# Kernel tuning notes

Hardware: AMD Instinct MI355X
Metric: run time of the kernel (lower is better)

## Reference

```python
import jax, jax.numpy as jnp
import numpy as np

B, T, C, H, K = 16, 8192, 256, 256, 7


def setup_inputs() -> dict:
    key = jax.random.key(0)
    ks = jax.random.split(key, 6)
    x = jax.random.normal(ks[0], (B, T, C), dtype=jnp.float32)
    # ragged lengths in [T//2, T]; padding_mask: True = padding (at tail)
    lengths = jax.random.randint(ks[1], (B,), T // 2, T + 1)
    padding_mask = jnp.arange(T)[None, :] >= lengths[:, None]
    w1 = jax.random.normal(ks[2], (H, C, K), dtype=jnp.float32) / np.sqrt(C * K)
    b1 = jnp.zeros((H,), jnp.float32)
    w2 = jax.random.normal(ks[3], (H, H, 3), dtype=jnp.float32) / np.sqrt(H * 3)
    b2 = jnp.zeros((H,), jnp.float32)
    w3 = jax.random.normal(ks[4], (2, H, 1), dtype=jnp.float32) / np.sqrt(H)
    b3 = jnp.zeros((2,), jnp.float32)
    return {"x": x, "padding_mask": padding_mask,
            "w1": w1, "b1": b1, "w2": w2, "b2": b2, "w3": w3, "b3": b3}


def _conv1d(h, w, b, pad):
    # h: (B, Cin, T), w: (Cout, Cin, K) torch OIW layout
    y = jax.lax.conv_general_dilated(h, w, (1,), [(pad, pad)],
                                     dimension_numbers=("NCH", "OIH", "NCH"))
    return y + b[None, :, None]


def _boundary_logits(x, w1, b1, w2, b2, w3, b3):
    # RebornSegmenter.forward (dropout is identity in eval)
    h = jnp.transpose(x, (0, 2, 1))            # (B, C, T)
    h = jax.nn.relu(_conv1d(h, w1, b1, K // 2))
    h = jax.nn.relu(_conv1d(h, w2, b2, 1))
    h = _conv1d(h, w3, b3, 0)                  # (B, 2, T)
    return jnp.transpose(h, (0, 2, 1))         # (B, T, 2)


def _segment_pool(xb, sid):
    # xb: (T, C), sid: (T,) in [0, T] (T == dropped/padding)
    sums = jax.ops.segment_sum(xb, sid, num_segments=T)
    cnt = jax.ops.segment_sum(jnp.ones((T,), xb.dtype), sid, num_segments=T)
    return sums, cnt


def reference(x, padding_mask, w1, b1, w2, b2, w3, b3):
    # pre_segment with deterministic=True (boundary = argmax of conv logits)
    boundary_logits = _boundary_logits(x, w1, b1, w2, b2, w3, b3)
    boundary = jnp.argmax(boundary_logits, axis=-1)            # (B, T)
    is_b = (boundary == 1) & (~padding_mask)
    # token t belongs to segment = number of boundaries in [0..t]
    seg_id = jnp.cumsum(is_b.astype(jnp.int32), axis=1)
    seg_id = jnp.where(padding_mask, T, seg_id)  # out-of-range -> dropped
    sums, cnt = jax.vmap(_segment_pool)(x, seg_id)             # (B,T,C),(B,T)
    # segment mean; empty segments -> 0 (output padded to T segments, jit-safe;
    # torch crops to max segment count, extra columns here are flagged padded)
    new_logits = jnp.where(cnt[..., None] > 0,
                           sums / jnp.maximum(cnt, 1.0)[..., None], 0.0)
    nb = jnp.sum(is_b, axis=1)
    n_valid = jnp.where(jnp.any(~padding_mask, axis=1), nb + 1, 0)
    new_pad = jnp.arange(T)[None, :] >= n_valid[:, None]       # (B, T)
    return new_logits, new_pad
```

## Files before the change

### kernel.cpp

```cpp
#include <hip/hip_runtime.h>
#include <cstdint>
#include <cstddef>

#define BSZ 16
#define T   8192
#define CDIM 256
#define HDIM 256
#define KW  7

constexpr int BT = BSZ * T;
constexpr float TAU = 2e-3f;
constexpr int RCAP = 8192;

typedef __attribute__((ext_vector_type(8))) short short8;
typedef _Float16 half8 __attribute__((ext_vector_type(8)));
typedef __attribute__((ext_vector_type(4))) float f32x4;

constexpr size_t B_W1T  = 0;
constexpr size_t B_W2T  = B_W1T + 1835008;
constexpr size_t B_V    = B_W2T + 786432;
constexpr size_t B_D    = B_V + 1024;
constexpr size_t B_ISB  = B_D + 524288;
constexpr size_t B_SID  = B_ISB + 524288;
constexpr size_t B_SST  = B_SID + 524288;
constexpr size_t B_SEN  = B_SST + 524288;
constexpr size_t B_NV   = B_SEN + 524288;
constexpr size_t B_UCT  = B_NV + 64;
constexpr size_t B_UL   = B_UCT + 16;
constexpr size_t B_ZERO = B_UL + 32768;
constexpr size_t B_W1B  = B_ZERO + 256;
constexpr size_t B_W2B  = B_W1B + 917504;
constexpr size_t B_H1F  = B_W2B + 393216;
constexpr size_t B_DSUM = B_H1F + 25165824;

__device__ __forceinline__ void gl_lds16(const void* g, void* l) {
    __builtin_amdgcn_global_load_lds(
        (const __attribute__((address_space(1))) unsigned int*)g,
        (__attribute__((address_space(3))) unsigned int*)l,
        16, 0, 0);
}

__device__ __forceinline__ unsigned short f16_rne(float f) {
    _Float16 h = (_Float16)f;
    return __builtin_bit_cast(unsigned short, h);
}


__global__ void repack_kernel(const float* __restrict__ w1, const float* __restrict__ w2,
                              const float* __restrict__ w3,
                              float* __restrict__ W1R, float* __restrict__ W2R,
                              float* __restrict__ v,
                              unsigned short* __restrict__ W1bL, unsigned short* __restrict__ W2bL)
{
    int idx = blockIdx.x * blockDim.x + threadIdx.x;
    int stride = gridDim.x * blockDim.x;
    for (int i = idx; i < HDIM * 1792; i += stride) {
        int h = i / 1792, kc = i % 1792, kw = kc >> 8, c = kc & 255;
        W1R[i] = w1[(size_t)h * 1792 + c * 7 + kw];
    }
    for (int i = idx; i < HDIM * 768; i += stride) {
        int h = i / 768, kc = i % 768, kw = kc >> 8, c = kc & 255;
        W2R[i] = w2[(size_t)h * 768 + c * 3 + kw];
    }
    for (int o = idx; o < 4 * 8 * 28 * 512; o += stride) {
        int e = o & 7, lane = (o >> 3) & 63;
        int su = o >> 9;
        int slot = su % 28, rest = su / 28;
        int cc = rest & 7, h0g = rest >> 3;
        int kw = slot >> 2, bq = slot & 3;
        int h = h0g * 64 + lane;
        int c = cc * 32 + bq * 8 + e;
        W1bL[o] = f16_rne(w1[(size_t)h * 1792 + c * 7 + kw]);
    }
    for (int o = idx; o < 4 * 8 * 12 * 512; o += stride) {
        int e = o & 7, lane = (o >> 3) & 63;
        int su = o >> 9;
        int slot = su % 12, rest = su / 12;
        int cc = rest & 7, h0g = rest >> 3;
        int kw = slot >> 2, bq = slot & 3;
        int h = h0g * 64 + lane;
        int c = cc * 32 + bq * 8 + e;
        W2bL[o] = f16_rne(w2[(size_t)h * 768 + c * 3 + kw]);
    }
    if (idx < HDIM) v[idx] = w3[HDIM + idx] - w3[idx];
}

__global__ __launch_bounds__(256) void xcast_kernel(const float* __restrict__ x,
                                                    unsigned short* __restrict__ xt)
{
    int j = blockIdx.x * 256 + threadIdx.x;
    int rin = j & 255, wid = (j >> 8) & 3, cc = (j >> 10) & 7, grp = (j >> 13) & 31, b = j >> 18;
    int t = grp * 256 + rin;
    int c0 = cc * 32 + wid * 8;
    const float* src = x + ((size_t)(b * T + t)) * 256 + c0;
    float4 a = *(const float4*)src;
    float4 bb = *(const float4*)(src + 4);
    short8 o;
    o[0] = (short)f16_rne(a.x); o[1] = (short)f16_rne(a.y);
    o[2] = (short)f16_rne(a.z); o[3] = (short)f16_rne(a.w);
    o[4] = (short)f16_rne(bb.x); o[5] = (short)f16_rne(bb.y);
    o[6] = (short)f16_rne(bb.z); o[7] = (short)f16_rne(bb.w);
    *(short8*)(xt + (size_t)j * 8) = o;
}

__device__ __forceinline__ void c1_stageA(const unsigned short* xt, const unsigned short* zerobuf,
                                          half8* Ab, int b, int t0, int cc, int lane, int wid)
{
    #pragma unroll
    for (int part = 0; part < 5; ++part) {
        int row = part * 64 + lane;
        int t = t0 + row - 3;
        const unsigned short* src = zerobuf;
        if (row < 262 && t >= 0 && t < T) {
            int grp = t >> 8, rin = t & 255;
            src = xt + ((size_t)((((b * 32 + grp) * 8 + cc) * 4 + wid) * 256 + rin)) * 8;
        }
        gl_lds16(src, &Ab[wid * 322 + part * 64]);
    }
}
__device__ __forceinline__ void c1_stageB(const unsigned short* WbL, half8* Bb,
                                          int hcc, int lane, int wid)
{
    #pragma unroll
    for (int s = 0; s < 7; ++s) {
        int slot = wid * 7 + s;
        const unsigned short* src = WbL + ((size_t)(hcc * 28 + slot)) * 512 + lane * 8;
        gl_lds16(src, &Bb[slot * 66]);
    }
}

__global__ __launch_bounds__(256, 3) void conv1_mfma(
    const unsigned short* __restrict__ xt,
    const unsigned short* __restrict__ WbL,
    const float* __restrict__ b1,
    const unsigned short* __restrict__ zerobuf,
    unsigned short* __restrict__ h1t)
{
    __shared__ half8 A8[4 * 322];
    __shared__ half8 B8[28 * 66];
    const int tid = threadIdx.x, lane = tid & 63, wid = tid >> 6;
    const int b  = blockIdx.x >> 5;
    const int grp = blockIdx.x & 31;
    const int t0 = grp << 8;
    const int h0 = blockIdx.y << 6;
    const int q = lane >> 4, l15 = lane & 15;

    f32x4 acc[4][4] = {};

    for (int cc = 0; cc < 8; ++cc) {
        __syncthreads();
        c1_stageA(xt, zerobuf, A8, b, t0, cc, lane, wid);
        c1_stageB(WbL, B8, blockIdx.y * 8 + cc, lane, wid);
        __syncthreads();
        #pragma unroll
        for (int kw = 0; kw < 7; ++kw) {
            half8 ah[4], bh[4];
            const int rbase = wid * 64 + l15 + kw;
            #pragma unroll
            for (int i = 0; i < 4; ++i) ah[i] = A8[q * 322 + rbase + i * 16];
            #pragma unroll
            for (int j = 0; j < 4; ++j) bh[j] = B8[(kw * 4 + q) * 66 + j * 16 + l15];
            #pragma unroll
            for (int i = 0; i < 4; ++i)
                #pragma unroll
                for (int j = 0; j < 4; ++j)
                    acc[i][j] = __builtin_amdgcn_mfma_f32_16x16x32_f16(ah[i], bh[j], acc[i][j], 0, 0, 0);
        }
    }
    #pragma unroll
    for (int j = 0; j < 4; ++j) {
        int h = h0 + j * 16 + l15;
        float bb = b1[h];
        int hcc = h >> 5, hwid = (h >> 3) & 3, he = h & 7;
        size_t hbase = ((size_t)(((b * 32 + grp) * 8 + hcc) * 4 + hwid)) * 2048 + he;
        #pragma unroll
        for (int i = 0; i < 4; ++i) {
            int rb = wid * 64 + i * 16 + q * 4;
            #pragma unroll
            for (int r = 0; r < 4; ++r)
                h1t[hbase + (size_t)(rb + r) * 8] = f16_rne(fmaxf(acc[i][j][r] + bb, 0.f));
        }
    }
}

__device__ __forceinline__ void c2_stageA(const unsigned short* ht, const unsigned short* zerobuf,
                                          half8* Ab, int b, int t0, int cc, int lane, int wid)
{
    #pragma unroll
    for (int part = 0; part < 5; ++part) {
        int row = part * 64 + lane;
        int t = t0 + row - 1;
        const unsigned short* src = zerobuf;
        if (row < 258 && t >= 0 && t < T) {
            int grp = t >> 8, rin = t & 255;
            src = ht + ((size_t)((((b * 32 + grp) * 8 + cc) * 4 + wid) * 256 + rin)) * 8;
        }
        gl_lds16(src, &Ab[wid * 322 + part * 64]);
    }
}
__device__ __forceinline__ void c2_stageB(const unsigned short* WbL, half8* Bb,
                                          int hcc, int lane, int wid)
{
    #pragma unroll
    for (int s = 0; s < 3; ++s) {
        int slot = wid * 3 + s;
        const unsigned short* src = WbL + ((size_t)(hcc * 12 + slot)) * 512 + lane * 8;
        gl_lds16(src, &Bb[slot * 66]);
    }
}

__global__ __launch_bounds__(256, 3) void conv2_mfma(
    const unsigned short* __restrict__ h1t,
    const unsigned short* __restrict__ WbL,
    const float* __restrict__ b2, const float* __restrict__ v,
    const unsigned short* __restrict__ zerobuf,
    float* __restrict__ dlog)
{
    __shared__ half8 A8[4 * 322];
    __shared__ half8 B8[12 * 66];
    const int tid = threadIdx.x, lane = tid & 63, wid = tid >> 6;
    const int b  = blockIdx.x >> 5;
    const int t0 = (blockIdx.x & 31) << 8;
    const int h0 = blockIdx.y << 6;
    const int q = lane >> 4, l15 = lane & 15;

    f32x4 acc[4][4] = {};

    for (int cc = 0; cc < 8; ++cc) {
        __syncthreads();
        c2_stageA(h1t, zerobuf, A8, b, t0, cc, lane, wid);
        c2_stageB(WbL, B8, blockIdx.y * 8 + cc, lane, wid);
        __syncthreads();
        #pragma unroll
        for (int kw = 0; kw < 3; ++kw) {
            half8 ah[4], bh[4];
            const int rbase = wid * 64 + l15 + kw;
            #pragma unroll
            for (int i = 0; i < 4; ++i) ah[i] = A8[q * 322 + rbase + i * 16];
            #pragma unroll
            for (int j = 0; j < 4; ++j) bh[j] = B8[(kw * 4 + q) * 66 + j * 16 + l15];
            #pragma unroll
            for (int i = 0; i < 4; ++i)
                #pragma unroll
                for (int j = 0; j < 4; ++j)
                    acc[i][j] = __builtin_amdgcn_mfma_f32_16x16x32_f16(ah[i], bh[j], acc[i][j], 0, 0, 0);
        }
    }
    float vv[4], bb[4];
    #pragma unroll
    for (int j = 0; j < 4; ++j) {
        int h = h0 + j * 16 + l15;
        vv[j] = v[h]; bb[j] = b2[h];
    }
    #pragma unroll
    for (int i = 0; i < 4; ++i) {
        int tb = t0 + wid * 64 + i * 16 + q * 4;
        #pragma unroll
        for (int r = 0; r < 4; ++r) {
            float s = 0.f;
            #pragma unroll
            for (int j = 0; j < 4; ++j)
                s += fmaxf(acc[i][j][r] + bb[j], 0.f) * vv[j];
            #pragma unroll
            for (int m = 1; m < 16; m <<= 1)
                s += __shfl_xor(s, m, 64);
            if (l15 == 0) atomicAdd(&dlog[b * T + tb + r], s);
        }
    }
}

__global__ void boundary_kernel(const float* __restrict__ d, const int* __restrict__ padmask,
                                const float* __restrict__ b3,
                                int* __restrict__ isb, int* __restrict__ ucount,
                                int* __restrict__ ulist)
{
    int bt = blockIdx.x * 256 + threadIdx.x;
    if (bt >= BT) return;
    int pad = padmask[bt];
    float dd = d[bt] + (b3[1] - b3[0]);
    isb[bt] = (pad == 0 && dd > 0.f) ? 1 : 0;
    if (pad == 0 && fabsf(dd) < TAU) {
        int slot = atomicAdd(ucount, 1);
        if (slot < RCAP) ulist[slot] = bt;
    }
}

__global__ __launch_bounds__(256) void recheck_h1(
    const float* __restrict__ x, const float* __restrict__ W1R,
    const float* __restrict__ b1, const float* __restrict__ zerof,
    const int* __restrict__ ulist, const int* __restrict__ ucount,
    float* __restrict__ h1f)
{
    __shared__ float xs[9 * CDIM];
    int n = *ucount; if (n > RCAP) n = RCAP;
    const int tid = threadIdx.x, lane = tid & 63, wid = tid >> 6;
    const int g = tid >> 4, l = tid & 15;
    const int nit = 4 * n;
    for (int item = blockIdx.x; item < nit; item += gridDim.x) {
        const int li = item >> 2, hc = item & 3;
        const int bt = ulist[li];
        const int b = bt >> 13, t = bt & (T - 1);
        __syncthreads();
        for (int r = wid; r < 9; r += 4) {
            int tt = t + r - 4;
            const float* src = (tt >= 0 && tt < T)
                ? x + (size_t)(b * T + tt) * CDIM + lane * 4 : zerof;
            gl_lds16(src, &xs[r * CDIM]);
        }
        __syncthreads();
        #pragma unroll
        for (int s = 0; s < 4; ++s) {
            const int h = hc * 64 + s * 16 + g;
            const float* wr = &W1R[(size_t)h * 1792];
            double p0 = 0.0, p1 = 0.0, p2 = 0.0;
            #pragma unroll 7
            for (int it = 0; it < 28; ++it) {
                const int e = it * 64 + l * 4;
                float4 w4 = *(const float4*)&wr[e];
                double w0 = (double)w4.x, w1v = (double)w4.y,
                       w2v = (double)w4.z, w3v = (double)w4.w;
                const float* x0 = &xs[e];
                p0 += w0 * (double)x0[0] + w1v * (double)x0[1]
                    + w2v * (double)x0[2] + w3v * (double)x0[3];
                const float* x1 = &xs[256 + e];
                p1 += w0 * (double)x1[0] + w1v * (double)x1[1]
                    + w2v * (double)x1[2] + w3v * (double)x1[3];
                const float* x2 = &xs[512 + e];
                p2 += w0 * (double)x2[0] + w1v * (double)x2[1]
                    + w2v * (double)x2[2] + w3v * (double)x2[3];
            }
            #pragma unroll
            for (int m = 1; m < 16; m <<= 1) {
                p0 += __shfl_xor(p0, m);
                p1 += __shfl_xor(p1, m);
                p2 += __shfl_xor(p2, m);
            }
            if (l == 0) {
                double bb = (double)b1[h];
                double a0 = bb + p0, a1 = bb + p1, a2 = bb + p2;
                float* o = &h1f[(size_t)li * 768];
                o[0 * 256 + h] = (t - 1 >= 0 && a0 > 0.0) ? (float)a0 : 0.f;
                o[1 * 256 + h] = (a1 > 0.0) ? (float)a1 : 0.f;
                o[2 * 256 + h] = (t + 1 < T && a2 > 0.0) ? (float)a2 : 0.f;
            }
        }
    }
}

__global__ __launch_bounds__(256) void recheck_h2(
    const float* __restrict__ h1f, const float* __restrict__ W2R,
    const float* __restrict__ b2, const float* __restrict__ w3,
    const int* __restrict__ ulist, const int* __restrict__ ucount,
    double* __restrict__ dsum)
{
    __shared__ float hs[768];
    __shared__ double red[64];
    int n = *ucount; if (n > RCAP) n = RCAP;
    const int tid = threadIdx.x, lane = tid & 63, wid = tid >> 6;
    const int g = tid >> 4, l = tid & 15;
    const int nit = 4 * n;
    for (int item = blockIdx.x; item < nit; item += gridDim.x) {
        const int li = item >> 2, hc = item & 3;
        __syncthreads();
        if (wid < 3)
            gl_lds16(h1f + (size_t)li * 768 + wid * 256 + lane * 4, &hs[wid * 256]);
        __syncthreads();
        #pragma unroll
        for (int s = 0; s < 4; ++s) {
            const int h = hc * 64 + s * 16 + g;
            const float* wr = &W2R[(size_t)h * 768];
            double c0 = 0.0;
            #pragma unroll
            for (int it = 0; it < 12; ++it) {
                const int e = it * 64 + l * 4;
                float4 w4 = *(const float4*)&wr[e];
                const float* hv = &hs[e];
                c0 += (double)w4.x * (double)hv[0] + (double)w4.y * (double)hv[1]
                    + (double)w4.z * (double)hv[2] + (double)w4.w * (double)hv[3];
            }
            #pragma unroll
            for (int m = 1; m < 16; m <<= 1) c0 += __shfl_xor(c0, m);
            if (l == 0) {
                double acc2 = (double)b2[h] + c0;
                double h2v = acc2 > 0.0 ? acc2 : 0.0;
                double vd = (double)w3[HDIM + h] - (double)w3[h];
                red[s * 16 + g] = vd * h2v;
            }
        }
        __syncthreads();
        if (tid < 32) red[tid] += red[tid + 32];
        __syncthreads();
        if (tid < 16) red[tid] += red[tid + 16];
        __syncthreads();
        if (tid == 0) {
            double ssum = 0.0;
            #pragma unroll
            for (int i = 0; i < 16; ++i) ssum += red[i];
            atomicAdd(&dsum[li], ssum);
        }
    }
}

__global__ void recheck_final(const double* __restrict__ dsum, const float* __restrict__ b3,
                              const int* __restrict__ ulist, const int* __restrict__ ucount,
                              int* __restrict__ isb)
{
    int n = *ucount; if (n > RCAP) n = RCAP;
    int li = blockIdx.x * 256 + threadIdx.x;
    if (li >= n) return;
    double dd = dsum[li] + ((double)b3[1] - (double)b3[0]);
    isb[ulist[li]] = (dd > 0.0) ? 1 : 0;
}

__global__ __launch_bounds__(1024) void scan_kernel(
    const int* __restrict__ isb, const int* __restrict__ padmask,
    int* __restrict__ sid, int* __restrict__ nvalid)
{
    __shared__ int ssum[1024];
    const int b = blockIdx.x, tid = threadIdx.x;
    const int base = b * T;
    int vals[8]; int s = 0;
    #pragma unroll
    for (int i = 0; i < 8; ++i) { vals[i] = isb[base + tid * 8 + i]; s += vals[i]; }
    ssum[tid] = s;
    __syncthreads();
    for (int off = 1; off < 1024; off <<= 1) {
        int add = (tid >= off) ? ssum[tid - off] : 0;
        __syncthreads();
        ssum[tid] += add;
        __syncthreads();
    }
    int run = ssum[tid] - s;
    #pragma unroll
    for (int i = 0; i < 8; ++i) {
        int t = tid * 8 + i;
        run += vals[i];
        sid[base + t] = (padmask[base + t] != 0) ? T : run;
    }
    if (tid == 1023) {
        int nb = ssum[1023];
        nvalid[b] = (padmask[base] == 0) ? (nb + 1) : 0;
    }
}

__global__ void segbounds_kernel(const int* __restrict__ sid, const int* __restrict__ padmask,
                                 int* __restrict__ sst, int* __restrict__ sen)
{
    int bt = blockIdx.x * 256 + threadIdx.x;
    if (bt >= BT) return;
    if (padmask[bt] != 0) return;
    int t = bt & (T - 1);
    int b = bt >> 13;
    int s = sid[bt];
    if (t == 0) {
        if (s < T) sst[b * T + s] = 0;
    } else if (s != sid[bt - 1]) {
        if (s < T) sst[b * T + s] = t;
    }
    bool last = (t == T - 1) || (padmask[bt + 1] != 0);
    if (s < T && (last || sid[bt + 1] != s)) sen[b * T + s] = t + 1;
}

__global__ __launch_bounds__(256) void pool_kernel(
    const float* __restrict__ x, const int* __restrict__ sst,
    const int* __restrict__ sen, const int* __restrict__ nvalid,
    float* __restrict__ out)
{
    int slot = blockIdx.x * 4 + (threadIdx.x >> 6);
    int lane = threadIdx.x & 63;
    int b = slot >> 13;
    int s = slot & (T - 1);
    int nv = nvalid[b];
    float4 res = make_float4(0.f, 0.f, 0.f, 0.f);
    if (s < nv) {
        int st = sst[slot], en = sen[slot];
        if (st >= 0 && en > st) {
            float4 a = make_float4(0.f, 0.f, 0.f, 0.f);
            const float* xp = &x[(size_t)(b * T + st) * CDIM + lane * 4];
            for (int t = st; t < en; ++t) {
                float4 xv = *(const float4*)xp;
                a.x += xv.x; a.y += xv.y; a.z += xv.z; a.w += xv.w;
                xp += CDIM;
            }
            float inv = 1.f / (float)(en - st);
            res = make_float4(a.x * inv, a.y * inv, a.z * inv, a.w * inv);
        }
    }
    *(float4*)&out[(size_t)slot * CDIM + lane * 4] = res;
    if (lane == 0) out[(size_t)BT * CDIM + slot] = (s < nv) ? 0.f : 1.f;
}

extern "C" void kernel_launch(void* const* d_in, const int* in_sizes, int n_in,
                              void* d_out, int out_size, void* d_ws, size_t ws_size,
                              hipStream_t stream)
{
    const float* x  = (const float*)d_in[0];
    const int* padmask = (const int*)d_in[1];
    const float* w1 = (const float*)d_in[2];
    const float* b1 = (const float*)d_in[3];
    const float* w2 = (const float*)d_in[4];
    const float* b2 = (const float*)d_in[5];
    const float* w3 = (const float*)d_in[6];
    const float* b3 = (const float*)d_in[7];

    char* ws = (char*)d_ws;
    float* W1R = (float*)(ws + B_W1T);
    float* W2R = (float*)(ws + B_W2T);
    float* v   = (float*)(ws + B_V);
    float* dlog = (float*)(ws + B_D);
    int* isb = (int*)(ws + B_ISB);
    int* sid = (int*)(ws + B_SID);
    int* sst = (int*)(ws + B_SST);
    int* sen = (int*)(ws + B_SEN);
    int* nv  = (int*)(ws + B_NV);
    int* uct = (int*)(ws + B_UCT);
    int* ul  = (int*)(ws + B_UL);
    unsigned short* zerobuf = (unsigned short*)(ws + B_ZERO);
    unsigned short* W1bL = (unsigned short*)(ws + B_W1B);
    unsigned short* W2bL = (unsigned short*)(ws + B_W2B);
    float* h1f = (float*)(ws + B_H1F);
    double* dsum = (double*)(ws + B_DSUM);

    float* out = (float*)d_out;
    unsigned short* h1t = (unsigned short*)out;
    unsigned short* xt  = h1t + (size_t)BT * 256;

    hipMemsetAsync(dlog, 0, BT * sizeof(float), stream);
    hipMemsetAsync(sst, 0xFF, BT * sizeof(int), stream);
    hipMemsetAsync(sen, 0xFF, BT * sizeof(int), stream);
    hipMemsetAsync(uct, 0, sizeof(int), stream);
    hipMemsetAsync(zerobuf, 0, 256, stream);
    hipMemsetAsync(dsum, 0, RCAP * sizeof(double), stream);

    repack_kernel<<<1024, 256, 0, stream>>>(w1, w2, w3, W1R, W2R, v, W1bL, W2bL);
    xcast_kernel<<<BT * 256 / (8 * 256), 256, 0, stream>>>(x, xt);
    conv1_mfma<<<dim3(BSZ * (T / 256), HDIM / 64), 256, 0, stream>>>(
        xt, W1bL, b1, zerobuf, h1t);
    conv2_mfma<<<dim3(BSZ * (T / 256), HDIM / 64), 256, 0, stream>>>(
        h1t, W2bL, b2, v, zerobuf, dlog);
    boundary_kernel<<<BT / 256, 256, 0, stream>>>(dlog, padmask, b3, isb, uct, ul);
    recheck_h1<<<4096, 256, 0, stream>>>(x, W1R, b1, (const float*)zerobuf, ul, uct, h1f);
    recheck_h2<<<4096, 256, 0, stream>>>(h1f, W2R, b2, w3, ul, uct, dsum);
    recheck_final<<<RCAP / 256, 256, 0, stream>>>(dsum, b3, ul, uct, isb);
    scan_kernel<<<BSZ, 1024, 0, stream>>>(isb, padmask, sid, nv);
    segbounds_kernel<<<BT / 256, 256, 0, stream>>>(sid, padmask, sst, sen);
    pool_kernel<<<BT / 4, 256, 0, stream>>>(x, sst, sen, nv, out);
}
```

Baseline: 586.2 us.

## Load conv weights directly into registers and remap blocks across XCDs

Measured after the change: 613.0 us. 4.6% more time.

```diff
diff --git a/kernel.cpp b/kernel.cpp
--- a/kernel.cpp
+++ b/kernel.cpp
@@ -118,16 +118,6 @@
         gl_lds16(src, &Ab[wid * 322 + part * 64]);
     }
 }
-__device__ __forceinline__ void c1_stageB(const unsigned short* WbL, half8* Bb,
-                                          int hcc, int lane, int wid)
-{
-    #pragma unroll
-    for (int s = 0; s < 7; ++s) {
-        int slot = wid * 7 + s;
-        const unsigned short* src = WbL + ((size_t)(hcc * 28 + slot)) * 512 + lane * 8;
-        gl_lds16(src, &Bb[slot * 66]);
-    }
-}
 
 __global__ __launch_bounds__(256, 3) void conv1_mfma(
     const unsigned short* __restrict__ xt,
@@ -137,34 +127,47 @@
     unsigned short* __restrict__ h1t)
 {
     __shared__ half8 A8[4 * 322];
-    __shared__ half8 B8[28 * 66];
     const int tid = threadIdx.x, lane = tid & 63, wid = tid >> 6;
-    const int b  = blockIdx.x >> 5;
-    const int grp = blockIdx.x & 31;
+    const int bid = blockIdx.x;
+    const int cid = (bid & 7) * 256 + (bid >> 3);
+    const int xcol = cid >> 2;
+    const int ycol = cid & 3;
+    const int b  = xcol >> 5;
+    const int grp = xcol & 31;
     const int t0 = grp << 8;
-    const int h0 = blockIdx.y << 6;
+    const int h0 = ycol << 6;
     const int q = lane >> 4, l15 = lane & 15;
+    const unsigned short* Wl0 = WbL + (size_t)(ycol * 8) * 28 * 512
+                                + (size_t)(q * 64 + l15) * 8;
 
     f32x4 acc[4][4] = {};
 
     for (int cc = 0; cc < 8; ++cc) {
         __syncthreads();
         c1_stageA(xt, zerobuf, A8, b, t0, cc, lane, wid);
-        c1_stageB(WbL, B8, blockIdx.y * 8 + cc, lane, wid);
+        const unsigned short* Wl = Wl0 + (size_t)cc * 14336;
+        half8 bh0[4], bh1[4];
+        #pragma unroll
+        for (int j = 0; j < 4; ++j) bh0[j] = *(const half8*)(Wl + j * 128);
         __syncthreads();
         #pragma unroll
         for (int kw = 0; kw < 7; ++kw) {
-            half8 ah[4], bh[4];
+            half8* cur = (kw & 1) ? bh1 : bh0;
+            half8* nxt = (kw & 1) ? bh0 : bh1;
+            if (kw < 6) {
+                #pragma unroll
+                for (int j = 0; j < 4; ++j)
+                    nxt[j] = *(const half8*)(Wl + (kw + 1) * 2048 + j * 128);
+            }
+            half8 ah[4];
             const int rbase = wid * 64 + l15 + kw;
             #pragma unroll
             for (int i = 0; i < 4; ++i) ah[i] = A8[q * 322 + rbase + i * 16];
-            #pragma unroll
-            for (int j = 0; j < 4; ++j) bh[j] = B8[(kw * 4 + q) * 66 + j * 16 + l15];
             #pragma unroll
             for (int i = 0; i < 4; ++i)
                 #pragma unroll
                 for (int j = 0; j < 4; ++j)
-                    acc[i][j] = __builtin_amdgcn_mfma_f32_16x16x32_f16(ah[i], bh[j], acc[i][j], 0, 0, 0);
+                    acc[i][j] = __builtin_amdgcn_mfma_f32_16x16x32_f16(ah[i], cur[j], acc[i][j], 0, 0, 0);
         }
     }
     #pragma unroll
@@ -198,16 +201,6 @@
         gl_lds16(src, &Ab[wid * 322 + part * 64]);
     }
 }
-__device__ __forceinline__ void c2_stageB(const unsigned short* WbL, half8* Bb,
-                                          int hcc, int lane, int wid)
-{
-    #pragma unroll
-    for (int s = 0; s < 3; ++s) {
-        int slot = wid * 3 + s;
-        const unsigned short* src = WbL + ((size_t)(hcc * 12 + slot)) * 512 + lane * 8;
-        gl_lds16(src, &Bb[slot * 66]);
-    }
-}
 
 __global__ __launch_bounds__(256, 3) void conv2_mfma(
     const unsigned short* __restrict__ h1t,
@@ -217,33 +210,46 @@
     float* __restrict__ dlog)
 {
     __shared__ half8 A8[4 * 322];
-    __shared__ half8 B8[12 * 66];
     const int tid = threadIdx.x, lane = tid & 63, wid = tid >> 6;
-    const int b  = blockIdx.x >> 5;
-    const int t0 = (blockIdx.x & 31) << 8;
-    const int h0 = blockIdx.y << 6;
+    const int bid = blockIdx.x;
+    const int cid = (bid & 7) * 256 + (bid >> 3);
+    const int xcol = cid >> 2;
+    const int ycol = cid & 3;
+    const int b  = xcol >> 5;
+    const int t0 = (xcol & 31) << 8;
+    const int h0 = ycol << 6;
     const int q = lane >> 4, l15 = lane & 15;
+    const unsigned short* Wl0 = WbL + (size_t)(ycol * 8) * 12 * 512
+                                + (size_t)(q * 64 + l15) * 8;
 
     f32x4 acc[4][4] = {};
 
     for (int cc = 0; cc < 8; ++cc) {
         __syncthreads();
         c2_stageA(h1t, zerobuf, A8, b, t0, cc, lane, wid);
-        c2_stageB(WbL, B8, blockIdx.y * 8 + cc, lane, wid);
+        const unsigned short* Wl = Wl0 + (size_t)cc * 6144;
+        half8 bh0[4], bh1[4];
+        #pragma unroll
+        for (int j = 0; j < 4; ++j) bh0[j] = *(const half8*)(Wl + j * 128);
         __syncthreads();
         #pragma unroll
         for (int kw = 0; kw < 3; ++kw) {
-            half8 ah[4], bh[4];
+            half8* cur = (kw & 1) ? bh1 : bh0;
+            half8* nxt = (kw & 1) ? bh0 : bh1;
+            if (kw < 2) {
+                #pragma unroll
+                for (int j = 0; j < 4; ++j)
+                    nxt[j] = *(const half8*)(Wl + (kw + 1) * 2048 + j * 128);
+            }
+            half8 ah[4];
             const int rbase = wid * 64 + l15 + kw;
             #pragma unroll
             for (int i = 0; i < 4; ++i) ah[i] = A8[q * 322 + rbase + i * 16];
-            #pragma unroll
-            for (int j = 0; j < 4; ++j) bh[j] = B8[(kw * 4 + q) * 66 + j * 16 + l15];
             #pragma unroll
             for (int i = 0; i < 4; ++i)
                 #pragma unroll
                 for (int j = 0; j < 4; ++j)
-                    acc[i][j] = __builtin_amdgcn_mfma_f32_16x16x32_f16(ah[i], bh[j], acc[i][j], 0, 0, 0);
+                    acc[i][j] = __builtin_amdgcn_mfma_f32_16x16x32_f16(ah[i], cur[j], acc[i][j], 0, 0, 0);
         }
     }
     float vv[4], bb[4];
@@ -534,10 +540,8 @@
 
     repack_kernel<<<1024, 256, 0, stream>>>(w1, w2, w3, W1R, W2R, v, W1bL, W2bL);
     xcast_kernel<<<BT * 256 / (8 * 256), 256, 0, stream>>>(x, xt);
-    conv1_mfma<<<dim3(BSZ * (T / 256), HDIM / 64), 256, 0, stream>>>(
-        xt, W1bL, b1, zerobuf, h1t);
-    conv2_mfma<<<dim3(BSZ * (T / 256), HDIM / 64), 256, 0, stream>>>(
-        h1t, W2bL, b2, v, zerobuf, dlog);
+    conv1_mfma<<<2048, 256, 0, stream>>>(xt, W1bL, b1, zerobuf, h1t);
+    conv2_mfma<<<2048, 256, 0, stream>>>(h1t, W2bL, b2, v, zerobuf, dlog);
     boundary_kernel<<<BT / 256, 256, 0, stream>>>(dlog, padmask, b3, isb, uct, ul);
     recheck_h1<<<4096, 256, 0, stream>>>(x, W1R, b1, (const float*)zerobuf, ul, uct, h1f);
     recheck_h2<<<4096, 256, 0, stream>>>(h1f, W2R, b2, w3, ul, uct, dsum);
```
